# Kernel tuning notes

Hardware: AMD Instinct MI355X
Metric: run time of the kernel (lower is better)

Reference implementation:

```python
import jax, jax.numpy as jnp
import numpy as np

B, N, C, H = 4, 1024, 1024, 16
D = C // H  # head_dim = 64


def setup_inputs() -> dict:
    key = jax.random.key(0)
    k1, k2, k3 = jax.random.split(key, 3)
    x = jax.random.normal(k1, (B, N, C), dtype=jnp.float32)
    Wqkv = jax.random.normal(k2, (3 * C, C), dtype=jnp.float32) * (C ** -0.5)
    Wproj = jax.random.normal(k3, (C, C), dtype=jnp.float32) * (C ** -0.5)
    bproj = jnp.zeros((C,), dtype=jnp.float32)
    epoch = 25  # selects mask_2 (window w=8) per the original branching
    return {"x": x, "Wqkv": Wqkv, "Wproj": Wproj, "bproj": bproj, "epoch": epoch}


def _band_mask(n, w):
    # get_attn_mask(N, w) == (|i - j| <= w) for every row (boundary cases included)
    idx = jnp.arange(n)
    return jnp.abs(idx[:, None] - idx[None, :]) <= w


def reference(x, Wqkv, Wproj, bproj, epoch):
    b, n, c = x.shape
    d = c // H
    # qkv linear (no bias), then the module's per-head interleaved split:
    # view(B,N,H,3d) -> permute(B,H,N,3d) -> tensor_split into q,k,v
    qkv = jnp.einsum('bnc,oc->bno', x, Wqkv)            # [B,N,3C]
    qkv = qkv.reshape(b, n, H, 3 * d).transpose(0, 2, 1, 3)  # [B,H,N,3d]
    q, k, v = jnp.split(qkv, 3, axis=-1)                # each [B,H,N,d]
    scale = d ** -0.5
    score = jnp.einsum('bhid,bhjd->bhij', q, k) * scale  # [B,H,N,N]
    if epoch is not None and epoch < 50:
        if epoch < 20:
            w = 6
        elif epoch < 30:
            w = 8
        elif epoch < 40:
            w = 10
        else:
            w = 12
        mask = _band_mask(n, w)  # [N,N] bool
        score = jnp.where(mask[None, None], score, jnp.float32(-1e9))
    attn = jax.nn.softmax(score, axis=-1)
    ctx = jnp.einsum('bhij,bhjd->bhid', attn, v)         # [B,H,N,d]
    ctx = ctx.transpose(0, 2, 1, 3).reshape(b, n, c)     # [B,N,C]
    out = jnp.einsum('bnc,oc->bno', ctx, Wproj) + bproj
    return out
```

## Files before the change

kernel.cpp:

```cpp
#include <hip/hip_runtime.h>
#include <hip/hip_bf16.h>


typedef __bf16 bf16x8_t __attribute__((ext_vector_type(8)));
typedef unsigned short u16x8_t __attribute__((ext_vector_type(8)));
typedef float f32x4_t __attribute__((ext_vector_type(4)));

__device__ __forceinline__ void load_lds16(const void* g, void* l) {
    __builtin_amdgcn_global_load_lds(
        (__attribute__((address_space(1))) void*)(g),
        (__attribute__((address_space(3))) void*)(l),
        16, 0, 0);
}

__global__ __launch_bounds__(256) void convert_all(
    const float* __restrict__ x, const float* __restrict__ wqkv,
    const float* __restrict__ wproj,
    __hip_bfloat16* __restrict__ xb, __hip_bfloat16* __restrict__ wqkvb,
    __hip_bfloat16* __restrict__ wprojb)
{
    const size_t t = (size_t)blockIdx.x * 256 + threadIdx.x;
    size_t i = t * 8;
    const float* src;
    __hip_bfloat16* dst;
    if (i < 4194304) {
        src = x; dst = xb;
    } else if (i < 4194304 + 3145728) {
        src = wqkv; dst = wqkvb; i -= 4194304;
    } else {
        src = wproj; dst = wprojb; i -= 4194304 + 3145728;
    }
    float4 v0 = *reinterpret_cast<const float4*>(src + i);
    float4 v1 = *reinterpret_cast<const float4*>(src + i + 4);
    union { u16x8_t v; __hip_bfloat16 h[8]; } u;
    u.h[0] = __float2bfloat16(v0.x); u.h[1] = __float2bfloat16(v0.y);
    u.h[2] = __float2bfloat16(v0.z); u.h[3] = __float2bfloat16(v0.w);
    u.h[4] = __float2bfloat16(v1.x); u.h[5] = __float2bfloat16(v1.y);
    u.h[6] = __float2bfloat16(v1.z); u.h[7] = __float2bfloat16(v1.w);
    *reinterpret_cast<u16x8_t*>(dst + i) = u.v;
}

__global__ __launch_bounds__(512, 2) void gemm1_qkv256(
    const __hip_bfloat16* __restrict__ A,
    const __hip_bfloat16* __restrict__ B,
    __hip_bfloat16* __restrict__ C)
{
    __shared__ __align__(16) char smem[135168];
    const int tid = threadIdx.x;
    const int m0 = blockIdx.y * 256, n0 = blockIdx.x * 256;
    const int wave = tid >> 6, lane = tid & 63;
    const int wr = wave >> 2, wc = wave & 3;
    const int lr = lane & 15, kg = lane >> 4;
    const int K = 1024, Nn = 3072;

    const int q0 = tid, q1 = tid + 512;
    const int ar0 = q0 >> 2, as0 = ((q0 & 3) ^ ((ar0 >> 1) & 3)) * 16;
    const int ar1 = q1 >> 2, as1 = ((q1 & 3) ^ ((ar1 >> 1) & 3)) * 16;
    const char* Asrc0 = (const char*)(A + (size_t)(m0 + ar0) * K) + as0;
    const char* Asrc1 = (const char*)(A + (size_t)(m0 + ar1) * K) + as1;
    const char* Bsrc0 = (const char*)(B + (size_t)(n0 + ar0) * K) + as0;
    const char* Bsrc1 = (const char*)(B + (size_t)(n0 + ar1) * K) + as1;

#define STAGE1(t) { const int sb_ = ((t) & 3) * 32768; const int ko_ = (t) * 64; \
    load_lds16(Asrc0 + ko_, smem + sb_ + q0 * 16);                               \
    load_lds16(Asrc1 + ko_, smem + sb_ + q1 * 16);                               \
    load_lds16(Bsrc0 + ko_, smem + sb_ + 16384 + q0 * 16);                       \
    load_lds16(Bsrc1 + ko_, smem + sb_ + 16384 + q1 * 16); }

    f32x4_t acc[8][4] = {};
    const int rsw = ((kg ^ ((lr >> 1) & 3)) * 16);
    const int arow = wr * 128 + lr;
    const int brow = wc * 64 + lr;

#define COMPUTE1(t) { const int sb_ = ((t) & 3) * 32768;                          \
    bf16x8_t a_[8], b_[4];                                                        \
    _Pragma("unroll") for (int mi = 0; mi < 8; ++mi)                              \
        a_[mi] = *(const bf16x8_t*)(smem + sb_ + (arow + mi * 16) * 64 + rsw);    \
    _Pragma("unroll") for (int ni = 0; ni < 4; ++ni)                              \
        b_[ni] = *(const bf16x8_t*)(smem + sb_ + 16384 + (brow + ni * 16) * 64 + rsw); \
    __builtin_amdgcn_s_setprio(1);                                                \
    _Pragma("unroll") for (int mi = 0; mi < 8; ++mi)                              \
    _Pragma("unroll") for (int ni = 0; ni < 4; ++ni)                              \
        acc[mi][ni] = __builtin_amdgcn_mfma_f32_16x16x32_bf16(                    \
            a_[mi], b_[ni], acc[mi][ni], 0, 0, 0);                                \
    __builtin_amdgcn_s_setprio(0); }

    STAGE1(0);
    STAGE1(1);
    for (int t = 0; t < 30; ++t) {
        STAGE1(t + 2);
        asm volatile("s_waitcnt vmcnt(8)" ::: "memory");
        __builtin_amdgcn_s_barrier();
        COMPUTE1(t);
    }
    asm volatile("s_waitcnt vmcnt(4)" ::: "memory");
    __builtin_amdgcn_s_barrier();
    COMPUTE1(30);
    asm volatile("s_waitcnt vmcnt(0)" ::: "memory");
    __builtin_amdgcn_s_barrier();
    COMPUTE1(31);
#undef STAGE1
#undef COMPUTE1

    __syncthreads();
    __hip_bfloat16* cl = (__hip_bfloat16*)smem;
#pragma unroll
    for (int mi = 0; mi < 8; ++mi)
#pragma unroll
        for (int ni = 0; ni < 4; ++ni)
#pragma unroll
            for (int r = 0; r < 4; ++r)
                cl[(wr * 128 + mi * 16 + kg * 4 + r) * 264 + wc * 64 + ni * 16 + lr] =
                    __float2bfloat16(acc[mi][ni][r]);
    __syncthreads();
#pragma unroll
    for (int c = 0; c < 16; ++c) {
        const int chunk = tid + c * 512;
        const int row = chunk >> 5, cc = chunk & 31;
        f32x4_t v = *(const f32x4_t*)(smem + row * 528 + cc * 16);
        *(f32x4_t*)((char*)C + ((size_t)(m0 + row) * Nn + n0) * 2 + cc * 16) = v;
    }
}

__global__ __launch_bounds__(256) void gemm2_proj(
    const __hip_bfloat16* __restrict__ A,
    const __hip_bfloat16* __restrict__ B,
    float* __restrict__ C,
    const float* __restrict__ bias)
{
    __shared__ char smem[16384];
    const int tid = threadIdx.x;
    const int m0 = blockIdx.y * 64, n0 = blockIdx.x * 128;
    const int wave = tid >> 6, lane = tid & 63;
    const int wr = wave >> 1, wc = wave & 1;
    const int lr = lane & 15, kg = lane >> 4;
    const int K = 1024, Nn = 1024;

    f32x4_t acc[2][4] = {};

    for (int k0 = 0; k0 < K; k0 += 32) {
        __syncthreads();
        {
            const int row = tid >> 2, cb = (tid & 3) * 8;
            load_lds16(A + (size_t)(m0 + row) * K + k0 + cb, smem + tid * 16);
        }
#pragma unroll
        for (int it = 0; it < 2; ++it) {
            const int c = tid + it * 256;
            const int row = c >> 2, cb = (c & 3) * 8;
            load_lds16(B + (size_t)(n0 + row) * K + k0 + cb,
                       smem + 4096 + c * 16);
        }
        __syncthreads();

        bf16x8_t a[2], b[4];
#pragma unroll
        for (int mi = 0; mi < 2; ++mi)
            a[mi] = *reinterpret_cast<const bf16x8_t*>(
                smem + ((wr * 32 + mi * 16 + lr) * 32 + kg * 8) * 2);
#pragma unroll
        for (int ni = 0; ni < 4; ++ni)
            b[ni] = *reinterpret_cast<const bf16x8_t*>(
                smem + 4096 + ((wc * 64 + ni * 16 + lr) * 32 + kg * 8) * 2);
#pragma unroll
        for (int mi = 0; mi < 2; ++mi)
#pragma unroll
            for (int ni = 0; ni < 4; ++ni)
                acc[mi][ni] = __builtin_amdgcn_mfma_f32_16x16x32_bf16(
                    a[mi], b[ni], acc[mi][ni], 0, 0, 0);
    }

    __syncthreads();
#pragma unroll
    for (int p = 0; p < 2; ++p) {
        if (p) __syncthreads();
        if (wr == p) {
#pragma unroll
            for (int mi = 0; mi < 2; ++mi)
#pragma unroll
                for (int ni = 0; ni < 4; ++ni) {
                    const int scol = wc * 64 + ni * 16 + lr;
#pragma unroll
                    for (int r = 0; r < 4; ++r) {
                        const int srow = mi * 16 + kg * 4 + r;
                        ((float*)smem)[srow * 128 + scol] = acc[mi][ni][r];
                    }
                }
        }
        __syncthreads();
#pragma unroll
        for (int cc = 0; cc < 4; ++cc) {
            const int chunk = tid + cc * 256;
            const int srow = chunk >> 5;
            const int sc = (chunk & 31) * 4;
            f32x4_t v = *reinterpret_cast<const f32x4_t*>(smem + chunk * 16);
            const f32x4_t bv = *reinterpret_cast<const f32x4_t*>(bias + n0 + sc);
            v += bv;
            *reinterpret_cast<f32x4_t*>(
                C + (size_t)(m0 + p * 32 + srow) * Nn + n0 + sc) = v;
        }
    }
}

__global__ __launch_bounds__(256) void attn_band_mfma(
    const __hip_bfloat16* __restrict__ qkv,
    __hip_bfloat16* __restrict__ ctx,
    const int* __restrict__ epoch_ptr)
{
    __shared__ __hip_bfloat16 P_lds[4][16 * 40];
    __shared__ __hip_bfloat16 V_lds[4][64 * 40];

    const int wave = threadIdx.x >> 6;
    const int lane = threadIdx.x & 63;
    const int lr = lane & 15, kg = lane >> 4;

    const int bid = blockIdx.x;
    const int tg = bid & 15;
    const int bh = bid >> 4;
    const int h = bh & 15, b = bh >> 4;
    const int i0 = (tg * 4 + wave) * 16;

    const int e = *epoch_ptr;
    int w;
    if      (e < 20) w = 6;
    else if (e < 30) w = 8;
    else if (e < 40) w = 10;
    else if (e < 50) w = 12;
    else             w = 1023;

    const size_t rowb = (size_t)b * 1024;
    const int hq = h * 192;

    bf16x8_t aq[2];
#pragma unroll
    for (int ks = 0; ks < 2; ++ks)
        aq[ks] = *(const bf16x8_t*)(qkv + (rowb + i0 + lr) * 3072 + hq + ks * 32 + kg * 8);

    float m[4] = {-1e30f, -1e30f, -1e30f, -1e30f};
    float l[4] = {0.f, 0.f, 0.f, 0.f};
    f32x4_t o[4] = {};

    int jlo = i0 - w;      if (jlo < 0) jlo = 0;
    int jhi = i0 + 15 + w; if (jhi > 1023) jhi = 1023;

    for (int p = (jlo >> 5); p <= (jhi >> 5); ++p) {
        const int kb = p * 32;

        const __hip_bfloat16* vbase0 = qkv + (rowb + kb + 2 * lr) * 3072 + hq + 128 + kg * 16;
        const __hip_bfloat16* vbase1 = vbase0 + 3072;
        u16x8_t va0 = *(const u16x8_t*)(vbase0);
        u16x8_t vb0 = *(const u16x8_t*)(vbase0 + 8);
        u16x8_t va1 = *(const u16x8_t*)(vbase1);
        u16x8_t vb1 = *(const u16x8_t*)(vbase1 + 8);

        f32x4_t s[2] = {};
#pragma unroll
        for (int t = 0; t < 2; ++t)
#pragma unroll
            for (int ks = 0; ks < 2; ++ks) {
                bf16x8_t bk = *(const bf16x8_t*)(
                    qkv + (rowb + kb + t * 16 + lr) * 3072 + hq + 64 + ks * 32 + kg * 8);
                s[t] = __builtin_amdgcn_mfma_f32_16x16x32_bf16(aq[ks], bk, s[t], 0, 0, 0);
            }

#pragma unroll
        for (int c = 0; c < 8; ++c) {
            unsigned int pk = (unsigned int)va0[c] | ((unsigned int)va1[c] << 16);
            *(unsigned int*)&V_lds[wave][(kg * 16 + c) * 40 + 2 * lr] = pk;
        }
#pragma unroll
        for (int c = 0; c < 8; ++c) {
            unsigned int pk = (unsigned int)vb0[c] | ((unsigned int)vb1[c] << 16);
            *(unsigned int*)&V_lds[wave][(kg * 16 + 8 + c) * 40 + 2 * lr] = pk;
        }

        float sv[2][4];
#pragma unroll
        for (int t = 0; t < 2; ++t)
#pragma unroll
            for (int r = 0; r < 4; ++r) {
                const int qi = i0 + kg * 4 + r;
                const int j  = kb + t * 16 + lr;
                int d = qi - j; if (d < 0) d = -d;
                sv[t][r] = (d <= w) ? s[t][r] * 0.125f : -1e30f;
            }

        float tm[4];
#pragma unroll
        for (int r = 0; r < 4; ++r) tm[r] = fmaxf(sv[0][r], sv[1][r]);
#pragma unroll
        for (int msk = 1; msk < 16; msk <<= 1)
#pragma unroll
            for (int r = 0; r < 4; ++r) tm[r] = fmaxf(tm[r], __shfl_xor(tm[r], msk));

        float sc[4], ps[4], pvv[2][4];
#pragma unroll
        for (int r = 0; r < 4; ++r) {
            const float mn = fmaxf(m[r], tm[r]);
            sc[r] = __expf(m[r] - mn);
            pvv[0][r] = __expf(sv[0][r] - mn);
            pvv[1][r] = __expf(sv[1][r] - mn);
            ps[r] = pvv[0][r] + pvv[1][r];
            m[r] = mn;
        }
#pragma unroll
        for (int msk = 1; msk < 16; msk <<= 1)
#pragma unroll
            for (int r = 0; r < 4; ++r) ps[r] += __shfl_xor(ps[r], msk);
#pragma unroll
        for (int r = 0; r < 4; ++r) l[r] = l[r] * sc[r] + ps[r];
#pragma unroll
        for (int ni = 0; ni < 4; ++ni)
#pragma unroll
            for (int r = 0; r < 4; ++r) o[ni][r] *= sc[r];

#pragma unroll
        for (int t = 0; t < 2; ++t)
#pragma unroll
            for (int r = 0; r < 4; ++r)
                P_lds[wave][(kg * 4 + r) * 40 + t * 16 + lr] =
                    __float2bfloat16(pvv[t][r]);

        bf16x8_t ap = *(const bf16x8_t*)&P_lds[wave][lr * 40 + kg * 8];
#pragma unroll
        for (int ni = 0; ni < 4; ++ni) {
            bf16x8_t bv = *(const bf16x8_t*)&V_lds[wave][(ni * 16 + lr) * 40 + kg * 8];
            o[ni] = __builtin_amdgcn_mfma_f32_16x16x32_bf16(ap, bv, o[ni], 0, 0, 0);
        }
    }

#pragma unroll
    for (int ni = 0; ni < 4; ++ni)
#pragma unroll
        for (int r = 0; r < 4; ++r)
            ctx[(rowb + i0 + kg * 4 + r) * 1024 + h * 64 + ni * 16 + lr] =
                __float2bfloat16(o[ni][r] / l[r]);
}

extern "C" void kernel_launch(void* const* d_in, const int* in_sizes, int n_in,
                              void* d_out, int out_size, void* d_ws, size_t ws_size,
                              hipStream_t stream)
{
    const float* x     = (const float*)d_in[0];
    const float* Wqkv  = (const float*)d_in[1];
    const float* Wproj = (const float*)d_in[2];
    const float* bproj = (const float*)d_in[3];
    const int*   epoch = (const int*)d_in[4];

    char* ws = (char*)d_ws;
    __hip_bfloat16* xb     = (__hip_bfloat16*)(ws);
    __hip_bfloat16* wqkvb  = (__hip_bfloat16*)(ws + 8388608);
    __hip_bfloat16* wprojb = (__hip_bfloat16*)(ws + 8388608 + 6291456);
    __hip_bfloat16* qkvb   = (__hip_bfloat16*)(ws + 16777216);
    __hip_bfloat16* ctxb   = (__hip_bfloat16*)(ws + 16777216 + 25165824);

    convert_all<<<4096, 256, 0, stream>>>(x, Wqkv, Wproj, xb, wqkvb, wprojb);

    gemm1_qkv256<<<dim3(3072 / 256, 4096 / 256), 512, 0, stream>>>(
        xb, wqkvb, qkvb);

    attn_band_mfma<<<1024, 256, 0, stream>>>(qkvb, ctxb, epoch);

    gemm2_proj<<<dim3(1024 / 128, 4096 / 64), 256, 0, stream>>>(
        ctxb, wprojb, (float*)d_out, bproj);
}
```

Before: 78.55 us.

## Stage shared K/V window in LDS per block and remap GEMM tiles per XCD

The attention kernel now cooperatively loads a 128-row K window (swizzled, async global-to-LDS) and a transposed V window once per block, shared by all four waves. Previously each wave reloaded K from global memory and re-transposed V per tile. Both GEMMs remap block indices so that tiles landing on the same XCD cover neighbouring output regions, which is meant to improve L2 reuse. The fixed 128-row window assumes a small band width, so the unbanded case (epoch >= 50) would index past the staged window.

```diff
diff --git a/kernel.cpp b/kernel.cpp
--- a/kernel.cpp
+++ b/kernel.cpp
@@ -47,7 +47,15 @@
 {
     __shared__ __align__(16) char smem[135168];
     const int tid = threadIdx.x;
-    const int m0 = blockIdx.y * 256, n0 = blockIdx.x * 256;
+
+    const int orig = blockIdx.y * 12 + blockIdx.x;
+    const int xcd = orig & 7, slot = orig >> 3;
+    const int hi = (slot >= 12) ? 1 : 0;
+    const int sup = xcd * 2 + hi;
+    const int local = slot - hi * 12;
+    const int m0 = ((sup & 3) * 4 + (local & 3)) * 256;
+    const int n0 = ((sup >> 2) * 3 + (local >> 2)) * 256;
+
     const int wave = tid >> 6, lane = tid & 63;
     const int wr = wave >> 2, wc = wave & 3;
     const int lr = lane & 15, kg = lane >> 4;
@@ -130,7 +138,9 @@
 {
     __shared__ char smem[16384];
     const int tid = threadIdx.x;
-    const int m0 = blockIdx.y * 64, n0 = blockIdx.x * 128;
+    const int orig = blockIdx.y * 8 + blockIdx.x;
+    const int wgid = (orig & 7) * 64 + (orig >> 3);
+    const int n0 = (wgid & 7) * 128, m0 = (wgid >> 3) * 64;
     const int wave = tid >> 6, lane = tid & 63;
     const int wr = wave >> 1, wc = wave & 1;
     const int lr = lane & 15, kg = lane >> 4;
@@ -207,18 +217,20 @@
     __hip_bfloat16* __restrict__ ctx,
     const int* __restrict__ epoch_ptr)
 {
+    __shared__ __align__(16) __hip_bfloat16 K_lds[128 * 64];
+    __shared__ __align__(16) __hip_bfloat16 V_lds[64 * 136];
     __shared__ __hip_bfloat16 P_lds[4][16 * 40];
-    __shared__ __hip_bfloat16 V_lds[4][64 * 40];
-
-    const int wave = threadIdx.x >> 6;
-    const int lane = threadIdx.x & 63;
+
+    const int tid = threadIdx.x;
+    const int wave = tid >> 6, lane = tid & 63;
     const int lr = lane & 15, kg = lane >> 4;
 
     const int bid = blockIdx.x;
     const int tg = bid & 15;
     const int bh = bid >> 4;
     const int h = bh & 15, b = bh >> 4;
-    const int i0 = (tg * 4 + wave) * 16;
+    const int base = tg * 64;
+    const int i0 = base + wave * 16;
 
     const int e = *epoch_ptr;
     int w;
@@ -231,10 +243,40 @@
     const size_t rowb = (size_t)b * 1024;
     const int hq = h * 192;
 
+#pragma unroll
+    for (int it = 0; it < 4; ++it) {
+        const int q = tid + it * 256;
+        const int row = q >> 3, s = q & 7;
+        const int c = s ^ (row & 7);
+        int gk = base - 32 + row;
+        gk = gk < 0 ? 0 : (gk > 1023 ? 1023 : gk);
+        load_lds16(qkv + (rowb + gk) * 3072 + hq + 64 + c * 8,
+                   (char*)K_lds + q * 16);
+    }
+    {
+        const int pr = tid & 63, dg = tid >> 6;
+        int gk0 = base - 32 + 2 * pr, gk1 = gk0 + 1;
+        gk0 = gk0 < 0 ? 0 : (gk0 > 1023 ? 1023 : gk0);
+        gk1 = gk1 < 0 ? 0 : (gk1 > 1023 ? 1023 : gk1);
+        const __hip_bfloat16* v0 = qkv + (rowb + gk0) * 3072 + hq + 128 + dg * 16;
+        const __hip_bfloat16* v1 = qkv + (rowb + gk1) * 3072 + hq + 128 + dg * 16;
+        u16x8_t a0 = *(const u16x8_t*)v0, b0 = *(const u16x8_t*)(v0 + 8);
+        u16x8_t a1 = *(const u16x8_t*)v1, b1 = *(const u16x8_t*)(v1 + 8);
+#pragma unroll
+        for (int c2 = 0; c2 < 8; ++c2) {
+            *(unsigned int*)&V_lds[(dg * 16 + c2) * 136 + 2 * pr] =
+                (unsigned int)a0[c2] | ((unsigned int)a1[c2] << 16);
+            *(unsigned int*)&V_lds[(dg * 16 + 8 + c2) * 136 + 2 * pr] =
+                (unsigned int)b0[c2] | ((unsigned int)b1[c2] << 16);
+        }
+    }
+
     bf16x8_t aq[2];
 #pragma unroll
     for (int ks = 0; ks < 2; ++ks)
         aq[ks] = *(const bf16x8_t*)(qkv + (rowb + i0 + lr) * 3072 + hq + ks * 32 + kg * 8);
+
+    __syncthreads();
 
     float m[4] = {-1e30f, -1e30f, -1e30f, -1e30f};
     float l[4] = {0.f, 0.f, 0.f, 0.f};
@@ -242,37 +284,22 @@
 
     int jlo = i0 - w;      if (jlo < 0) jlo = 0;
     int jhi = i0 + 15 + w; if (jhi > 1023) jhi = 1023;
+    const int t0 = (base >> 5) - 1;
 
     for (int p = (jlo >> 5); p <= (jhi >> 5); ++p) {
         const int kb = p * 32;
-
-        const __hip_bfloat16* vbase0 = qkv + (rowb + kb + 2 * lr) * 3072 + hq + 128 + kg * 16;
-        const __hip_bfloat16* vbase1 = vbase0 + 3072;
-        u16x8_t va0 = *(const u16x8_t*)(vbase0);
-        u16x8_t vb0 = *(const u16x8_t*)(vbase0 + 8);
-        u16x8_t va1 = *(const u16x8_t*)(vbase1);
-        u16x8_t vb1 = *(const u16x8_t*)(vbase1 + 8);
-
-        f32x4_t s[2] = {};
+        const int tl = p - t0;
+
+        f32x4_t s2[2] = {};
 #pragma unroll
         for (int t = 0; t < 2; ++t)
 #pragma unroll
             for (int ks = 0; ks < 2; ++ks) {
+                const int lkr = tl * 32 + t * 16 + lr;
                 bf16x8_t bk = *(const bf16x8_t*)(
-                    qkv + (rowb + kb + t * 16 + lr) * 3072 + hq + 64 + ks * 32 + kg * 8);
-                s[t] = __builtin_amdgcn_mfma_f32_16x16x32_bf16(aq[ks], bk, s[t], 0, 0, 0);
+                    (char*)K_lds + lkr * 128 + (((ks * 4 + kg) ^ (lr & 7)) * 16));
+                s2[t] = __builtin_amdgcn_mfma_f32_16x16x32_bf16(aq[ks], bk, s2[t], 0, 0, 0);
             }
-
-#pragma unroll
-        for (int c = 0; c < 8; ++c) {
-            unsigned int pk = (unsigned int)va0[c] | ((unsigned int)va1[c] << 16);
-            *(unsigned int*)&V_lds[wave][(kg * 16 + c) * 40 + 2 * lr] = pk;
-        }
-#pragma unroll
-        for (int c = 0; c < 8; ++c) {
-            unsigned int pk = (unsigned int)vb0[c] | ((unsigned int)vb1[c] << 16);
-            *(unsigned int*)&V_lds[wave][(kg * 16 + 8 + c) * 40 + 2 * lr] = pk;
-        }
 
         float sv[2][4];
 #pragma unroll
@@ -282,7 +309,7 @@
                 const int qi = i0 + kg * 4 + r;
                 const int j  = kb + t * 16 + lr;
                 int d = qi - j; if (d < 0) d = -d;
-                sv[t][r] = (d <= w) ? s[t][r] * 0.125f : -1e30f;
+                sv[t][r] = (d <= w) ? s2[t][r] * 0.125f : -1e30f;
             }
 
         float tm[4];
@@ -324,7 +351,7 @@
         bf16x8_t ap = *(const bf16x8_t*)&P_lds[wave][lr * 40 + kg * 8];
 #pragma unroll
         for (int ni = 0; ni < 4; ++ni) {
-            bf16x8_t bv = *(const bf16x8_t*)&V_lds[wave][(ni * 16 + lr) * 40 + kg * 8];
+            bf16x8_t bv = *(const bf16x8_t*)&V_lds[(ni * 16 + lr) * 136 + tl * 32 + kg * 8];
             o[ni] = __builtin_amdgcn_mfma_f32_16x16x32_bf16(ap, bv, o[ni], 0, 0, 0);
         }
     }
```

Result: faster. 76.25 us (-2.9%).
